# Kernel optimization log

Measured on AMD Instinct MI355X. Metric: run time of the kernel, lower is better.

## Reference

```python
import jax, jax.numpy as jnp
import numpy as np

N_NODES, N_EDGES, D, B, K, M = 100000, 500000, 172, 500, 10, 1000
MSG = 4 * D  # 2*memory_dim + edge_dim + time_dim = 688


def setup_inputs() -> dict:
    ks = jax.random.split(jax.random.key(0), 34)
    rn = lambda k, s, sc=0.05: jax.random.normal(k, s, jnp.float32) * sc
    ri = lambda k, s, hi: jax.random.randint(k, s, 0, hi, dtype=jnp.int32)
    ru = lambda k, s, sc=1000.0: jax.random.uniform(k, s, dtype=jnp.float32) * sc
    return {
        "node_feats": rn(ks[0], (N_NODES, D)),
        "edge_feats": rn(ks[1], (N_EDGES, D)),
        "memory": rn(ks[2], (N_NODES, D)),
        "time_w": rn(ks[3], (D,), 1.0),
        "time_b": rn(ks[4], (D,), 1.0),
        "W_ih": rn(ks[5], (3 * D, MSG)),
        "W_hh": rn(ks[6], (3 * D, D)),
        "b_ih": rn(ks[7], (3 * D,)),
        "b_hh": rn(ks[8], (3 * D,)),
        "lin1_w": rn(ks[9], (2, 3 * D, D)),
        "lin1_b": rn(ks[10], (2, D)),
        "lin2_w": rn(ks[11], (2, 3 * D, D)),
        "lin2_b": rn(ks[12], (2, D)),
        "aff_w1": rn(ks[13], (2 * D, D)),
        "aff_b1": rn(ks[14], (D,)),
        "aff_w2": rn(ks[15], (D, 1)),
        "aff_b2": rn(ks[16], (1,)),
        "dec_w": rn(ks[17], (D, D)),
        "dec_b": rn(ks[18], (D,)),
        "edge_times": ru(ks[19], (B,)),
        "nbr1_t": ru(ks[20], (3 * B, K)),
        "nbr2_t": ru(ks[21], (3 * B * K, K)),
        "msgs": rn(ks[22], (M, MSG)),
        "msg_times": ru(ks[23], (M,)),
        "src": ri(ks[24], (B,), N_NODES),
        "dst": ri(ks[25], (B,), N_NODES),
        "neg": ri(ks[26], (B,), N_NODES),
        "edge_idxs": ri(ks[27], (B,), N_EDGES),
        "nbr1_ids": ri(ks[28], (3 * B, K), N_NODES),
        "nbr1_eidx": ri(ks[29], (3 * B, K), N_EDGES),
        "nbr2_ids": ri(ks[30], (3 * B * K, K), N_NODES),
        "nbr2_eidx": ri(ks[31], (3 * B * K, K), N_EDGES),
        "msg_node_ids": jnp.arange(M, dtype=jnp.int32),  # unique nodes with pending messages
    }


def _time_enc(t, w, b):
    # TGN TimeEncode: cos(t * w + b), broadcast over last dim D
    return jnp.cos(t[..., None] * w + b)


def _gru(x, h, W_ih, W_hh, b_ih, b_hh):
    # torch.nn.GRUCell math
    gi = x @ W_ih.T + b_ih
    gh = h @ W_hh.T + b_hh
    ir, iz, ig = jnp.split(gi, 3, -1)
    hr, hz, hg = jnp.split(gh, 3, -1)
    r = jax.nn.sigmoid(ir + hr)
    z = jax.nn.sigmoid(iz + hz)
    g = jnp.tanh(ig + r * hg)
    return (1.0 - z) * g + z * h


def _agg(l, src_feat, ts, nbr_emb, nbr_t, edge_f, tw, tb, l1w, l1b, l2w, l2b):
    # GraphSumEmbedding.aggregate for layer index l (0-based = n_layer-1)
    dt = _time_enc(ts[:, None] - nbr_t, tw, tb)                 # [N,K,D]
    nf = jnp.concatenate([nbr_emb, dt, edge_f], -1)             # [N,K,3D]
    h = jax.nn.relu((nf @ l1w[l] + l1b[l]).sum(1))              # sum over K neighbors -> [N,D]
    st = _time_enc(jnp.zeros_like(ts), tw, tb)                  # time-embedding of delta 0
    s = jnp.concatenate([h, src_feat, st], -1)                  # [N,3D]
    return s @ l2w[l] + l2b[l]


def reference(node_feats, edge_feats, memory, time_w, time_b, W_ih, W_hh, b_ih, b_hh,
              lin1_w, lin1_b, lin2_w, lin2_b, aff_w1, aff_b1, aff_w2, aff_b2,
              dec_w, dec_b, edge_times, nbr1_t, nbr2_t, msgs, msg_times,
              src, dst, neg, edge_idxs, nbr1_ids, nbr1_eidx, nbr2_ids, nbr2_eidx,
              msg_node_ids):
    b, k = src.shape[0], nbr1_ids.shape[1]
    d = node_feats.shape[1]
    # 1) get_updated_memory: GRU update of nodes with aggregated-last messages, scatter into bank
    h_new = _gru(msgs, memory[msg_node_ids], W_ih, W_hh, b_ih, b_hh)
    mem = memory.at[msg_node_ids].set(h_new)
    feat0 = lambda n: mem[n] + node_feats[n]  # layer-0 embedding = memory + raw features
    # 2) two-layer graph-sum temporal embedding over concat(src,dst,neg)
    nodes = jnp.concatenate([src, dst, neg])                    # [3B]
    ts = jnp.concatenate([edge_times, edge_times, edge_times])  # [3B]
    n1 = nbr1_ids.reshape(-1)                                   # [3B*K]
    ts1 = jnp.repeat(ts, k)                                     # [3B*K]
    emb1 = _agg(0, feat0(n1), ts1, feat0(nbr2_ids), nbr2_t,
                edge_feats[nbr2_eidx], time_w, time_b, lin1_w, lin1_b, lin2_w, lin2_b)
    emb2 = _agg(1, feat0(nodes), ts, emb1.reshape(-1, k, d), nbr1_t,
                edge_feats[nbr1_eidx], time_w, time_b, lin1_w, lin1_b, lin2_w, lin2_b)
    s_emb, d_emb, g_emb = emb2[:b], emb2[b:2 * b], emb2[2 * b:]
    # 3) affinity (MergeLayer) scores + MLP decode + raw feature gather
    def merge(x1, x2):
        h = jax.nn.relu(jnp.concatenate([x1, x2], -1) @ aff_w1 + aff_b1)
        return (h @ aff_w2 + aff_b2).reshape(-1)
    pos_prob = jax.nn.sigmoid(merge(s_emb, d_emb))
    neg_prob = jax.nn.sigmoid(merge(s_emb, g_emb))
    decode = jnp.concatenate([s_emb, d_emb], 0) @ dec_w + dec_b
    raw = jnp.concatenate([node_feats[src], node_feats[dst]], 0)
    return (pos_prob, neg_prob, decode, raw)
```

## Files before the change

### kernel.cpp

```cpp
#include <hip/hip_runtime.h>

#define DD   172
#define TK   516
#define BB   500
#define KK   10
#define MM   1000
#define MSGW 688
#define NR1  1500
#define NR2  15000

__device__ __forceinline__ float sigm(float x){ return 1.f / (1.f + expf(-x)); }

__global__ void k_tr(const float* __restrict__ in, float* __restrict__ out,
                     int R, int C){
  __shared__ float tile[32][33];
  int c0 = blockIdx.x * 32, r0 = blockIdx.y * 32;
  int tx = threadIdx.x, ty = threadIdx.y;
  for (int i = ty; i < 32; i += 8){
    int r = r0 + i, c = c0 + tx;
    if (r < R && c < C) tile[i][tx] = in[(size_t)r*C + c];
  }
  __syncthreads();
  for (int i = ty; i < 32; i += 8){
    int c = c0 + i, r = r0 + tx;
    if (c < C && r < R) out[(size_t)c*R + r] = tile[tx][i];
  }
}

__global__ void k_gru2(const float* __restrict__ msgs, float* memory,
                       const float* __restrict__ WT_ih,
                       const float* __restrict__ WT_hh,
                       const float* __restrict__ b_ih, const float* __restrict__ b_hh,
                       const int* __restrict__ ids){
  int t = threadIdx.x;
  int r0 = blockIdx.x * 2;
  __shared__ __align__(16) float xT[MSGW][2];
  __shared__ __align__(16) float hT[DD][2];
  int s0 = ids[r0], s1 = ids[r0 + 1];
  for (int c = t; c < MSGW; c += 192){
    xT[c][0] = msgs[(size_t)r0*MSGW + c];
    xT[c][1] = msgs[(size_t)(r0+1)*MSGW + c];
  }
  if (t < DD){
    hT[t][0] = memory[(size_t)s0*DD + t];
    hT[t][1] = memory[(size_t)s1*DD + t];
  }
  __syncthreads();
  if (t < DD){
    float gi00 = b_ih[t],      gi01 = gi00;
    float gi10 = b_ih[DD+t],   gi11 = gi10;
    float gi20 = b_ih[2*DD+t], gi21 = gi20;
    #pragma unroll 4
    for (int c = 0; c < MSGW; c++){
      const float* wr = WT_ih + (size_t)c*TK;
      float w0 = wr[t], w1 = wr[DD+t], w2 = wr[2*DD+t];
      float2 xv = *reinterpret_cast<const float2*>(&xT[c][0]);
      gi00 = fmaf(xv.x, w0, gi00); gi01 = fmaf(xv.y, w0, gi01);
      gi10 = fmaf(xv.x, w1, gi10); gi11 = fmaf(xv.y, w1, gi11);
      gi20 = fmaf(xv.x, w2, gi20); gi21 = fmaf(xv.y, w2, gi21);
    }
    float gh00 = b_hh[t],      gh01 = gh00;
    float gh10 = b_hh[DD+t],   gh11 = gh10;
    float gh20 = b_hh[2*DD+t], gh21 = gh20;
    #pragma unroll 4
    for (int c = 0; c < DD; c++){
      const float* wr = WT_hh + (size_t)c*TK;
      float w0 = wr[t], w1 = wr[DD+t], w2 = wr[2*DD+t];
      float2 hv = *reinterpret_cast<const float2*>(&hT[c][0]);
      gh00 = fmaf(hv.x, w0, gh00); gh01 = fmaf(hv.y, w0, gh01);
      gh10 = fmaf(hv.x, w1, gh10); gh11 = fmaf(hv.y, w1, gh11);
      gh20 = fmaf(hv.x, w2, gh20); gh21 = fmaf(hv.y, w2, gh21);
    }
    {
      float r_ = sigm(gi00 + gh00);
      float z  = sigm(gi10 + gh10);
      float g  = tanhf(gi20 + r_*gh20);
      memory[(size_t)s0*DD + t] = (1.f - z)*g + z*hT[t][0];
    }
    {
      float r_ = sigm(gi01 + gh01);
      float z  = sigm(gi11 + gh11);
      float g  = tanhf(gi21 + r_*gh21);
      memory[(size_t)s1*DD + t] = (1.f - z)*g + z*hT[t][1];
    }
  }
}

__global__ void k_c2(const float* __restrict__ time_b, const float* __restrict__ lin2_w,
                     const float* __restrict__ lin2_b, float* __restrict__ consts){
  int l = blockIdx.x, j = threadIdx.x;
  __shared__ float cb[DD];
  if (j < DD) cb[j] = cosf(time_b[j]);
  __syncthreads();
  if (j < DD){
    float acc = lin2_b[(size_t)l*DD + j];
    const float* W = lin2_w + (size_t)l*TK*DD;
    for (int d = 0; d < DD; d++) acc = fmaf(cb[d], W[(size_t)(2*DD + d)*DD + j], acc);
    consts[l*DD + j] = acc;
  }
}

__global__ void k_hop2(const float* __restrict__ nf, const float* __restrict__ ef,
                       const float* __restrict__ mem, const float* __restrict__ tw,
                       const float* __restrict__ tb, const float* __restrict__ et,
                       const float* __restrict__ n2t, const int* __restrict__ n2i,
                       const int* __restrict__ n2e, const int* __restrict__ n1i,
                       const float* __restrict__ l1w, const float* __restrict__ l2w,
                       const float* __restrict__ l1b, const float* __restrict__ consts,
                       float* __restrict__ emb1){
  int t = threadIdx.x;
  int r0 = blockIdx.x * 8;
  __shared__ __align__(16) float S[TK][8];
  __shared__ __align__(16) float H[2*DD][8];
  __shared__ int   I2[8*KK], E2[8*KK], SID[8];
  __shared__ float T2[8*KK];
  if (t < 8*KK){
    int r = r0 + t/KK, k = t % KK;
    I2[t] = n2i[(size_t)r*KK + k];
    E2[t] = n2e[(size_t)r*KK + k];
    T2[t] = n2t[(size_t)r*KK + k];
  }
  if (t >= 96 && t < 104) SID[t-96] = n1i[r0 + (t-96)];
  __syncthreads();
  if (t < DD){
    float w = tw[t], b = tb[t];
    for (int rr = 0; rr < 8; rr++){
      int r = r0 + rr;
      float ts = et[(r/KK) % BB];
      float sn = 0.f, sd = 0.f, se = 0.f;
      #pragma unroll
      for (int k = 0; k < KK; k++){
        int id = I2[rr*KK + k];
        int e  = E2[rr*KK + k];
        float dt = ts - T2[rr*KK + k];
        sn += mem[(size_t)id*DD + t] + nf[(size_t)id*DD + t];
        sd += cosf(dt*w + b);
        se += ef[(size_t)e*DD + t];
      }
      S[t][rr] = sn; S[DD + t][rr] = sd; S[2*DD + t][rr] = se;
      int sid = SID[rr];
      H[DD + t][rr] = mem[(size_t)sid*DD + t] + nf[(size_t)sid*DD + t];
    }
  }
  __syncthreads();
  if (t < DD){
    float acc[8];
    float b10 = 10.f * l1b[t];
    #pragma unroll
    for (int rr = 0; rr < 8; rr++) acc[rr] = b10;
    const float* Wp = l1w + t;
    #pragma unroll 4
    for (int c = 0; c < TK; c++){
      float wv = Wp[(size_t)c*DD];
      float4 a = *reinterpret_cast<const float4*>(&S[c][0]);
      float4 q = *reinterpret_cast<const float4*>(&S[c][4]);
      acc[0] = fmaf(a.x, wv, acc[0]); acc[1] = fmaf(a.y, wv, acc[1]);
      acc[2] = fmaf(a.z, wv, acc[2]); acc[3] = fmaf(a.w, wv, acc[3]);
      acc[4] = fmaf(q.x, wv, acc[4]); acc[5] = fmaf(q.y, wv, acc[5]);
      acc[6] = fmaf(q.z, wv, acc[6]); acc[7] = fmaf(q.w, wv, acc[7]);
    }
    #pragma unroll
    for (int rr = 0; rr < 8; rr++) H[t][rr] = fmaxf(acc[rr], 0.f);
  }
  __syncthreads();
  if (t < DD){
    float acc[8];
    float c2 = consts[t];
    #pragma unroll
    for (int rr = 0; rr < 8; rr++) acc[rr] = c2;
    const float* Wp = l2w + t;
    #pragma unroll 4
    for (int c = 0; c < 2*DD; c++){
      float wv = Wp[(size_t)c*DD];
      float4 a = *reinterpret_cast<const float4*>(&H[c][0]);
      float4 q = *reinterpret_cast<const float4*>(&H[c][4]);
      acc[0] = fmaf(a.x, wv, acc[0]); acc[1] = fmaf(a.y, wv, acc[1]);
      acc[2] = fmaf(a.z, wv, acc[2]); acc[3] = fmaf(a.w, wv, acc[3]);
      acc[4] = fmaf(q.x, wv, acc[4]); acc[5] = fmaf(q.y, wv, acc[5]);
      acc[6] = fmaf(q.z, wv, acc[6]); acc[7] = fmaf(q.w, wv, acc[7]);
    }
    #pragma unroll
    for (int rr = 0; rr < 8; rr++) emb1[(size_t)(r0+rr)*DD + t] = acc[rr];
  }
}

__global__ void k_hop1(const float* __restrict__ nf, const float* __restrict__ ef,
                       const float* __restrict__ mem, const float* __restrict__ tw,
                       const float* __restrict__ tb, const float* __restrict__ et,
                       const float* __restrict__ n1t, const int* __restrict__ n1e,
                       const int* __restrict__ src, const int* __restrict__ dst,
                       const int* __restrict__ neg, const float* __restrict__ emb1,
                       const float* __restrict__ l1w, const float* __restrict__ l2w,
                       const float* __restrict__ l1b, const float* __restrict__ consts,
                       float* __restrict__ emb2){
  int t = threadIdx.x;
  int r0 = blockIdx.x * 8;
  __shared__ __align__(16) float S[TK][8];
  __shared__ __align__(16) float H[2*DD][8];
  __shared__ int   E1[8*KK], SID[8];
  __shared__ float T1[8*KK];
  if (t < 8*KK){
    int q = r0 + t/KK; if (q >= NR1) q = NR1 - 1;
    int k = t % KK;
    E1[t] = n1e[(size_t)q*KK + k];
    T1[t] = n1t[(size_t)q*KK + k];
  }
  if (t >= 96 && t < 104){
    int q = r0 + (t - 96); if (q >= NR1) q = NR1 - 1;
    SID[t-96] = (q < BB) ? src[q] : (q < 2*BB ? dst[q - BB] : neg[q - 2*BB]);
  }
  __syncthreads();
  if (t < DD){
    float w = tw[t], b = tb[t];
    for (int rr = 0; rr < 8; rr++){
      int q = r0 + rr; if (q >= NR1) q = NR1 - 1;
      float ts = et[q % BB];
      float sn = 0.f, sd = 0.f, se = 0.f;
      #pragma unroll
      for (int k = 0; k < KK; k++){
        int e = E1[rr*KK + k];
        float dt = ts - T1[rr*KK + k];
        sn += emb1[((size_t)q*KK + k)*DD + t];
        sd += cosf(dt*w + b);
        se += ef[(size_t)e*DD + t];
      }
      S[t][rr] = sn; S[DD + t][rr] = sd; S[2*DD + t][rr] = se;
      int sid = SID[rr];
      H[DD + t][rr] = mem[(size_t)sid*DD + t] + nf[(size_t)sid*DD + t];
    }
  }
  __syncthreads();
  if (t < DD){
    float acc[8];
    float b10 = 10.f * l1b[t];
    #pragma unroll
    for (int rr = 0; rr < 8; rr++) acc[rr] = b10;
    const float* Wp = l1w + t;
    #pragma unroll 4
    for (int c = 0; c < TK; c++){
      float wv = Wp[(size_t)c*DD];
      float4 a = *reinterpret_cast<const float4*>(&S[c][0]);
      float4 q = *reinterpret_cast<const float4*>(&S[c][4]);
      acc[0] = fmaf(a.x, wv, acc[0]); acc[1] = fmaf(a.y, wv, acc[1]);
      acc[2] = fmaf(a.z, wv, acc[2]); acc[3] = fmaf(a.w, wv, acc[3]);
      acc[4] = fmaf(q.x, wv, acc[4]); acc[5] = fmaf(q.y, wv, acc[5]);
      acc[6] = fmaf(q.z, wv, acc[6]); acc[7] = fmaf(q.w, wv, acc[7]);
    }
    #pragma unroll
    for (int rr = 0; rr < 8; rr++) H[t][rr] = fmaxf(acc[rr], 0.f);
  }
  __syncthreads();
  if (t < DD){
    float acc[8];
    float c2 = consts[DD + t];
    #pragma unroll
    for (int rr = 0; rr < 8; rr++) acc[rr] = c2;
    const float* Wp = l2w + t;
    #pragma unroll 4
    for (int c = 0; c < 2*DD; c++){
      float wv = Wp[(size_t)c*DD];
      float4 a = *reinterpret_cast<const float4*>(&H[c][0]);
      float4 q = *reinterpret_cast<const float4*>(&H[c][4]);
      acc[0] = fmaf(a.x, wv, acc[0]); acc[1] = fmaf(a.y, wv, acc[1]);
      acc[2] = fmaf(a.z, wv, acc[2]); acc[3] = fmaf(a.w, wv, acc[3]);
      acc[4] = fmaf(q.x, wv, acc[4]); acc[5] = fmaf(q.y, wv, acc[5]);
      acc[6] = fmaf(q.z, wv, acc[6]); acc[7] = fmaf(q.w, wv, acc[7]);
    }
    #pragma unroll
    for (int rr = 0; rr < 8; rr++){
      int q = r0 + rr;
      if (q < NR1) emb2[(size_t)q*DD + t] = acc[rr];
    }
  }
}

__global__ void k_merge(const float* __restrict__ emb2, const float* __restrict__ aff_w1,
                        const float* __restrict__ aff_b1, const float* __restrict__ aff_w2,
                        const float* __restrict__ aff_b2, float* __restrict__ out){
  int idx = blockIdx.x;
  int which = idx / BB, r = idx % BB;
  int t = threadIdx.x;
  __shared__ float x1[DD], x2[DD], hs[DD];
  if (t < DD){
    x1[t] = emb2[(size_t)r*DD + t];
    x2[t] = emb2[(size_t)(which == 0 ? BB + r : 2*BB + r)*DD + t];
  }
  __syncthreads();
  if (t < DD){
    float acc = aff_b1[t];
    for (int c = 0; c < DD; c++) acc = fmaf(x1[c], aff_w1[(size_t)c*DD + t], acc);
    for (int c = 0; c < DD; c++) acc = fmaf(x2[c], aff_w1[(size_t)(DD + c)*DD + t], acc);
    hs[t] = fmaxf(acc, 0.f) * aff_w2[t];
  }
  __syncthreads();
  if (t < 64){
    float s = hs[t] + hs[t + 64];
    if (t < DD - 128) s += hs[t + 128];
    #pragma unroll
    for (int off = 32; off > 0; off >>= 1) s += __shfl_down(s, off, 64);
    if (t == 0) out[which*BB + r] = sigm(s + aff_b2[0]);
  }
}

__global__ void k_dec(const float* __restrict__ emb2, const float* __restrict__ dec_w,
                      const float* __restrict__ dec_b, float* __restrict__ out){
  int t = threadIdx.x;
  int r0 = blockIdx.x * 8;
  if (t < DD){
    float acc[8];
    float bj = dec_b[t];
    #pragma unroll
    for (int rr = 0; rr < 8; rr++) acc[rr] = bj;
    for (int c = 0; c < DD; c++){
      float wv = dec_w[(size_t)c*DD + t];
      #pragma unroll
      for (int rr = 0; rr < 8; rr++)
        acc[rr] = fmaf(emb2[(size_t)(r0+rr)*DD + c], wv, acc[rr]);
    }
    #pragma unroll
    for (int rr = 0; rr < 8; rr++) out[(size_t)(r0+rr)*DD + t] = acc[rr];
  }
}

__global__ void k_raw(const float* __restrict__ node_feats, const int* __restrict__ src,
                      const int* __restrict__ dst, float* __restrict__ out){
  int q = blockIdx.x, t = threadIdx.x;
  int id = (q < BB) ? src[q] : dst[q - BB];
  if (t < DD) out[(size_t)q*DD + t] = node_feats[(size_t)id*DD + t];
}

extern "C" void kernel_launch(void* const* d_in, const int* in_sizes, int n_in,
                              void* d_out, int out_size, void* d_ws, size_t ws_size,
                              hipStream_t stream){
  (void)in_sizes; (void)n_in; (void)out_size; (void)ws_size;
  const float* node_feats = (const float*)d_in[0];
  const float* edge_feats = (const float*)d_in[1];
  float*       memory     = (float*)d_in[2];
  const float* time_w     = (const float*)d_in[3];
  const float* time_b     = (const float*)d_in[4];
  const float* W_ih       = (const float*)d_in[5];
  const float* W_hh       = (const float*)d_in[6];
  const float* b_ih       = (const float*)d_in[7];
  const float* b_hh       = (const float*)d_in[8];
  const float* lin1_w     = (const float*)d_in[9];
  const float* lin1_b     = (const float*)d_in[10];
  const float* lin2_w     = (const float*)d_in[11];
  const float* lin2_b     = (const float*)d_in[12];
  const float* aff_w1     = (const float*)d_in[13];
  const float* aff_b1     = (const float*)d_in[14];
  const float* aff_w2     = (const float*)d_in[15];
  const float* aff_b2     = (const float*)d_in[16];
  const float* dec_w      = (const float*)d_in[17];
  const float* dec_b      = (const float*)d_in[18];
  const float* edge_times = (const float*)d_in[19];
  const float* nbr1_t     = (const float*)d_in[20];
  const float* nbr2_t     = (const float*)d_in[21];
  const float* msgs       = (const float*)d_in[22];
  const int* src        = (const int*)d_in[24];
  const int* dst        = (const int*)d_in[25];
  const int* neg        = (const int*)d_in[26];
  const int* nbr1_ids   = (const int*)d_in[28];
  const int* nbr1_eidx  = (const int*)d_in[29];
  const int* nbr2_ids   = (const int*)d_in[30];
  const int* nbr2_eidx  = (const int*)d_in[31];
  const int* msg_ids    = (const int*)d_in[32];
  float* out = (float*)d_out;

  float* consts = (float*)d_ws;
  float* emb1   = (float*)((char*)d_ws + 2048);
  float* emb2   = emb1 + (size_t)NR2*DD;
  float* WT_ih  = emb1;
  float* WT_hh  = WT_ih + (size_t)MSGW*TK;

  k_tr  <<<dim3((MSGW+31)/32, (TK+31)/32), dim3(32,8), 0, stream>>>(W_ih, WT_ih, TK, MSGW);
  k_tr  <<<dim3((DD+31)/32,   (TK+31)/32), dim3(32,8), 0, stream>>>(W_hh, WT_hh, TK, DD);
  k_gru2<<<MM/2, 192, 0, stream>>>(msgs, memory, WT_ih, WT_hh, b_ih, b_hh, msg_ids);
  k_c2  <<<2, 192, 0, stream>>>(time_b, lin2_w, lin2_b, consts);
  k_hop2<<<NR2/8, 192, 0, stream>>>(node_feats, edge_feats, memory, time_w, time_b,
                                    edge_times, nbr2_t, nbr2_ids, nbr2_eidx, nbr1_ids,
                                    lin1_w, lin2_w, lin1_b, consts, emb1);
  k_hop1<<<(NR1+7)/8, 192, 0, stream>>>(node_feats, edge_feats, memory, time_w, time_b,
                                        edge_times, nbr1_t, nbr1_eidx, src, dst, neg,
                                        emb1, lin1_w + (size_t)TK*DD, lin2_w + (size_t)TK*DD,
                                        lin1_b + DD, consts, emb2);
  k_merge<<<2*BB, 192, 0, stream>>>(emb2, aff_w1, aff_b1, aff_w2, aff_b2, out);
  k_dec <<<MM/8, 192, 0, stream>>>(emb2, dec_w, dec_b, out + 2*BB);
  k_raw <<<MM, 192, 0, stream>>>(node_feats, src, dst, out + 2*BB + (size_t)MM*DD);
}
```

Baseline: 993.7 us.

## Batch weight loads ahead of FMAs, shrink shared memory, stage decoder inputs

Result: faster. 938.5 us (-5.6%).

```diff
diff --git a/kernel.cpp b/kernel.cpp
--- a/kernel.cpp
+++ b/kernel.cpp
@@ -50,26 +50,38 @@
     float gi00 = b_ih[t],      gi01 = gi00;
     float gi10 = b_ih[DD+t],   gi11 = gi10;
     float gi20 = b_ih[2*DD+t], gi21 = gi20;
-    #pragma unroll 4
-    for (int c = 0; c < MSGW; c++){
-      const float* wr = WT_ih + (size_t)c*TK;
-      float w0 = wr[t], w1 = wr[DD+t], w2 = wr[2*DD+t];
-      float2 xv = *reinterpret_cast<const float2*>(&xT[c][0]);
-      gi00 = fmaf(xv.x, w0, gi00); gi01 = fmaf(xv.y, w0, gi01);
-      gi10 = fmaf(xv.x, w1, gi10); gi11 = fmaf(xv.y, w1, gi11);
-      gi20 = fmaf(xv.x, w2, gi20); gi21 = fmaf(xv.y, w2, gi21);
+    for (int c0 = 0; c0 < MSGW; c0 += 8){
+      float w0[8], w1[8], w2[8]; float2 xv[8];
+      #pragma unroll
+      for (int u = 0; u < 8; u++){
+        const float* wr = WT_ih + (size_t)(c0+u)*TK;
+        w0[u] = wr[t]; w1[u] = wr[DD+t]; w2[u] = wr[2*DD+t];
+        xv[u] = *reinterpret_cast<const float2*>(&xT[c0+u][0]);
+      }
+      #pragma unroll
+      for (int u = 0; u < 8; u++){
+        gi00 = fmaf(xv[u].x, w0[u], gi00); gi01 = fmaf(xv[u].y, w0[u], gi01);
+        gi10 = fmaf(xv[u].x, w1[u], gi10); gi11 = fmaf(xv[u].y, w1[u], gi11);
+        gi20 = fmaf(xv[u].x, w2[u], gi20); gi21 = fmaf(xv[u].y, w2[u], gi21);
+      }
     }
     float gh00 = b_hh[t],      gh01 = gh00;
     float gh10 = b_hh[DD+t],   gh11 = gh10;
     float gh20 = b_hh[2*DD+t], gh21 = gh20;
-    #pragma unroll 4
-    for (int c = 0; c < DD; c++){
-      const float* wr = WT_hh + (size_t)c*TK;
-      float w0 = wr[t], w1 = wr[DD+t], w2 = wr[2*DD+t];
-      float2 hv = *reinterpret_cast<const float2*>(&hT[c][0]);
-      gh00 = fmaf(hv.x, w0, gh00); gh01 = fmaf(hv.y, w0, gh01);
-      gh10 = fmaf(hv.x, w1, gh10); gh11 = fmaf(hv.y, w1, gh11);
-      gh20 = fmaf(hv.x, w2, gh20); gh21 = fmaf(hv.y, w2, gh21);
+    for (int c0 = 0; c0 < DD; c0 += 4){
+      float w0[4], w1[4], w2[4]; float2 hv[4];
+      #pragma unroll
+      for (int u = 0; u < 4; u++){
+        const float* wr = WT_hh + (size_t)(c0+u)*TK;
+        w0[u] = wr[t]; w1[u] = wr[DD+t]; w2[u] = wr[2*DD+t];
+        hv[u] = *reinterpret_cast<const float2*>(&hT[c0+u][0]);
+      }
+      #pragma unroll
+      for (int u = 0; u < 4; u++){
+        gh00 = fmaf(hv[u].x, w0[u], gh00); gh01 = fmaf(hv[u].y, w0[u], gh01);
+        gh10 = fmaf(hv[u].x, w1[u], gh10); gh11 = fmaf(hv[u].y, w1[u], gh11);
+        gh20 = fmaf(hv[u].x, w2[u], gh20); gh21 = fmaf(hv[u].y, w2[u], gh21);
+      }
     }
     {
       float r_ = sigm(gi00 + gh00);
@@ -94,8 +106,14 @@
   __syncthreads();
   if (j < DD){
     float acc = lin2_b[(size_t)l*DD + j];
-    const float* W = lin2_w + (size_t)l*TK*DD;
-    for (int d = 0; d < DD; d++) acc = fmaf(cb[d], W[(size_t)(2*DD + d)*DD + j], acc);
+    const float* W = lin2_w + (size_t)l*TK*DD + (size_t)2*DD*DD + j;
+    for (int d0 = 0; d0 < DD; d0 += 4){
+      float wv[4];
+      #pragma unroll
+      for (int u = 0; u < 4; u++) wv[u] = W[(size_t)(d0+u)*DD];
+      #pragma unroll
+      for (int u = 0; u < 4; u++) acc = fmaf(cb[d0+u], wv[u], acc);
+    }
     consts[l*DD + j] = acc;
   }
 }
@@ -111,7 +129,7 @@
   int t = threadIdx.x;
   int r0 = blockIdx.x * 8;
   __shared__ __align__(16) float S[TK][8];
-  __shared__ __align__(16) float H[2*DD][8];
+  __shared__ __align__(16) float Hhi[DD][8];
   __shared__ int   I2[8*KK], E2[8*KK], SID[8];
   __shared__ float T2[8*KK];
   if (t < 8*KK){
@@ -127,57 +145,97 @@
     for (int rr = 0; rr < 8; rr++){
       int r = r0 + rr;
       float ts = et[(r/KK) % BB];
-      float sn = 0.f, sd = 0.f, se = 0.f;
+      float vm[KK], vn[KK], ve[KK], vt[KK];
       #pragma unroll
       for (int k = 0; k < KK; k++){
         int id = I2[rr*KK + k];
         int e  = E2[rr*KK + k];
-        float dt = ts - T2[rr*KK + k];
-        sn += mem[(size_t)id*DD + t] + nf[(size_t)id*DD + t];
-        sd += cosf(dt*w + b);
-        se += ef[(size_t)e*DD + t];
+        vm[k] = mem[(size_t)id*DD + t];
+        vn[k] = nf[(size_t)id*DD + t];
+        ve[k] = ef[(size_t)e*DD + t];
+        vt[k] = T2[rr*KK + k];
+      }
+      float sn = 0.f, sd = 0.f, se = 0.f;
+      #pragma unroll
+      for (int k = 0; k < KK; k++){
+        sn += vm[k] + vn[k];
+        sd += cosf((ts - vt[k])*w + b);
+        se += ve[k];
       }
       S[t][rr] = sn; S[DD + t][rr] = sd; S[2*DD + t][rr] = se;
       int sid = SID[rr];
-      H[DD + t][rr] = mem[(size_t)sid*DD + t] + nf[(size_t)sid*DD + t];
-    }
-  }
-  __syncthreads();
-  if (t < DD){
-    float acc[8];
+      Hhi[t][rr] = mem[(size_t)sid*DD + t] + nf[(size_t)sid*DD + t];
+    }
+  }
+  __syncthreads();
+  float acc[8];
+  if (t < DD){
     float b10 = 10.f * l1b[t];
     #pragma unroll
     for (int rr = 0; rr < 8; rr++) acc[rr] = b10;
     const float* Wp = l1w + t;
-    #pragma unroll 4
-    for (int c = 0; c < TK; c++){
-      float wv = Wp[(size_t)c*DD];
-      float4 a = *reinterpret_cast<const float4*>(&S[c][0]);
-      float4 q = *reinterpret_cast<const float4*>(&S[c][4]);
-      acc[0] = fmaf(a.x, wv, acc[0]); acc[1] = fmaf(a.y, wv, acc[1]);
-      acc[2] = fmaf(a.z, wv, acc[2]); acc[3] = fmaf(a.w, wv, acc[3]);
-      acc[4] = fmaf(q.x, wv, acc[4]); acc[5] = fmaf(q.y, wv, acc[5]);
-      acc[6] = fmaf(q.z, wv, acc[6]); acc[7] = fmaf(q.w, wv, acc[7]);
-    }
-    #pragma unroll
-    for (int rr = 0; rr < 8; rr++) H[t][rr] = fmaxf(acc[rr], 0.f);
-  }
-  __syncthreads();
-  if (t < DD){
-    float acc[8];
+    for (int c0 = 0; c0 < TK; c0 += 4){
+      float wv[4]; float4 a[4], q[4];
+      #pragma unroll
+      for (int u = 0; u < 4; u++){
+        wv[u] = Wp[(size_t)(c0+u)*DD];
+        a[u] = *reinterpret_cast<const float4*>(&S[c0+u][0]);
+        q[u] = *reinterpret_cast<const float4*>(&S[c0+u][4]);
+      }
+      #pragma unroll
+      for (int u = 0; u < 4; u++){
+        acc[0]=fmaf(a[u].x,wv[u],acc[0]); acc[1]=fmaf(a[u].y,wv[u],acc[1]);
+        acc[2]=fmaf(a[u].z,wv[u],acc[2]); acc[3]=fmaf(a[u].w,wv[u],acc[3]);
+        acc[4]=fmaf(q[u].x,wv[u],acc[4]); acc[5]=fmaf(q[u].y,wv[u],acc[5]);
+        acc[6]=fmaf(q[u].z,wv[u],acc[6]); acc[7]=fmaf(q[u].w,wv[u],acc[7]);
+      }
+    }
+  }
+  __syncthreads();
+  if (t < DD){
+    float4 h0, h1;
+    h0.x=fmaxf(acc[0],0.f); h0.y=fmaxf(acc[1],0.f); h0.z=fmaxf(acc[2],0.f); h0.w=fmaxf(acc[3],0.f);
+    h1.x=fmaxf(acc[4],0.f); h1.y=fmaxf(acc[5],0.f); h1.z=fmaxf(acc[6],0.f); h1.w=fmaxf(acc[7],0.f);
+    *reinterpret_cast<float4*>(&S[t][0]) = h0;
+    *reinterpret_cast<float4*>(&S[t][4]) = h1;
+  }
+  __syncthreads();
+  if (t < DD){
     float c2 = consts[t];
     #pragma unroll
     for (int rr = 0; rr < 8; rr++) acc[rr] = c2;
     const float* Wp = l2w + t;
-    #pragma unroll 4
-    for (int c = 0; c < 2*DD; c++){
-      float wv = Wp[(size_t)c*DD];
-      float4 a = *reinterpret_cast<const float4*>(&H[c][0]);
-      float4 q = *reinterpret_cast<const float4*>(&H[c][4]);
-      acc[0] = fmaf(a.x, wv, acc[0]); acc[1] = fmaf(a.y, wv, acc[1]);
-      acc[2] = fmaf(a.z, wv, acc[2]); acc[3] = fmaf(a.w, wv, acc[3]);
-      acc[4] = fmaf(q.x, wv, acc[4]); acc[5] = fmaf(q.y, wv, acc[5]);
-      acc[6] = fmaf(q.z, wv, acc[6]); acc[7] = fmaf(q.w, wv, acc[7]);
+    for (int c0 = 0; c0 < DD; c0 += 4){
+      float wv[4]; float4 a[4], q[4];
+      #pragma unroll
+      for (int u = 0; u < 4; u++){
+        wv[u] = Wp[(size_t)(c0+u)*DD];
+        a[u] = *reinterpret_cast<const float4*>(&S[c0+u][0]);
+        q[u] = *reinterpret_cast<const float4*>(&S[c0+u][4]);
+      }
+      #pragma unroll
+      for (int u = 0; u < 4; u++){
+        acc[0]=fmaf(a[u].x,wv[u],acc[0]); acc[1]=fmaf(a[u].y,wv[u],acc[1]);
+        acc[2]=fmaf(a[u].z,wv[u],acc[2]); acc[3]=fmaf(a[u].w,wv[u],acc[3]);
+        acc[4]=fmaf(q[u].x,wv[u],acc[4]); acc[5]=fmaf(q[u].y,wv[u],acc[5]);
+        acc[6]=fmaf(q[u].z,wv[u],acc[6]); acc[7]=fmaf(q[u].w,wv[u],acc[7]);
+      }
+    }
+    for (int c0 = 0; c0 < DD; c0 += 4){
+      float wv[4]; float4 a[4], q[4];
+      #pragma unroll
+      for (int u = 0; u < 4; u++){
+        wv[u] = Wp[(size_t)(DD+c0+u)*DD];
+        a[u] = *reinterpret_cast<const float4*>(&Hhi[c0+u][0]);
+        q[u] = *reinterpret_cast<const float4*>(&Hhi[c0+u][4]);
+      }
+      #pragma unroll
+      for (int u = 0; u < 4; u++){
+        acc[0]=fmaf(a[u].x,wv[u],acc[0]); acc[1]=fmaf(a[u].y,wv[u],acc[1]);
+        acc[2]=fmaf(a[u].z,wv[u],acc[2]); acc[3]=fmaf(a[u].w,wv[u],acc[3]);
+        acc[4]=fmaf(q[u].x,wv[u],acc[4]); acc[5]=fmaf(q[u].y,wv[u],acc[5]);
+        acc[6]=fmaf(q[u].z,wv[u],acc[6]); acc[7]=fmaf(q[u].w,wv[u],acc[7]);
+      }
     }
     #pragma unroll
     for (int rr = 0; rr < 8; rr++) emb1[(size_t)(r0+rr)*DD + t] = acc[rr];
@@ -196,7 +254,7 @@
   int t = threadIdx.x;
   int r0 = blockIdx.x * 8;
   __shared__ __align__(16) float S[TK][8];
-  __shared__ __align__(16) float H[2*DD][8];
+  __shared__ __align__(16) float Hhi[DD][8];
   __shared__ int   E1[8*KK], SID[8];
   __shared__ float T1[8*KK];
   if (t < 8*KK){
@@ -215,56 +273,95 @@
     for (int rr = 0; rr < 8; rr++){
       int q = r0 + rr; if (q >= NR1) q = NR1 - 1;
       float ts = et[q % BB];
-      float sn = 0.f, sd = 0.f, se = 0.f;
+      float v1[KK], ve[KK], vt[KK];
       #pragma unroll
       for (int k = 0; k < KK; k++){
         int e = E1[rr*KK + k];
-        float dt = ts - T1[rr*KK + k];
-        sn += emb1[((size_t)q*KK + k)*DD + t];
-        sd += cosf(dt*w + b);
-        se += ef[(size_t)e*DD + t];
+        v1[k] = emb1[((size_t)q*KK + k)*DD + t];
+        ve[k] = ef[(size_t)e*DD + t];
+        vt[k] = T1[rr*KK + k];
+      }
+      float sn = 0.f, sd = 0.f, se = 0.f;
+      #pragma unroll
+      for (int k = 0; k < KK; k++){
+        sn += v1[k];
+        sd += cosf((ts - vt[k])*w + b);
+        se += ve[k];
       }
       S[t][rr] = sn; S[DD + t][rr] = sd; S[2*DD + t][rr] = se;
       int sid = SID[rr];
-      H[DD + t][rr] = mem[(size_t)sid*DD + t] + nf[(size_t)sid*DD + t];
-    }
-  }
-  __syncthreads();
-  if (t < DD){
-    float acc[8];
+      Hhi[t][rr] = mem[(size_t)sid*DD + t] + nf[(size_t)sid*DD + t];
+    }
+  }
+  __syncthreads();
+  float acc[8];
+  if (t < DD){
     float b10 = 10.f * l1b[t];
     #pragma unroll
     for (int rr = 0; rr < 8; rr++) acc[rr] = b10;
     const float* Wp = l1w + t;
-    #pragma unroll 4
-    for (int c = 0; c < TK; c++){
-      float wv = Wp[(size_t)c*DD];
-      float4 a = *reinterpret_cast<const float4*>(&S[c][0]);
-      float4 q = *reinterpret_cast<const float4*>(&S[c][4]);
-      acc[0] = fmaf(a.x, wv, acc[0]); acc[1] = fmaf(a.y, wv, acc[1]);
-      acc[2] = fmaf(a.z, wv, acc[2]); acc[3] = fmaf(a.w, wv, acc[3]);
-      acc[4] = fmaf(q.x, wv, acc[4]); acc[5] = fmaf(q.y, wv, acc[5]);
-      acc[6] = fmaf(q.z, wv, acc[6]); acc[7] = fmaf(q.w, wv, acc[7]);
-    }
-    #pragma unroll
-    for (int rr = 0; rr < 8; rr++) H[t][rr] = fmaxf(acc[rr], 0.f);
-  }
-  __syncthreads();
-  if (t < DD){
-    float acc[8];
+    for (int c0 = 0; c0 < TK; c0 += 4){
+      float wv[4]; float4 a[4], q[4];
+      #pragma unroll
+      for (int u = 0; u < 4; u++){
+        wv[u] = Wp[(size_t)(c0+u)*DD];
+        a[u] = *reinterpret_cast<const float4*>(&S[c0+u][0]);
+        q[u] = *reinterpret_cast<const float4*>(&S[c0+u][4]);
+      }
+      #pragma unroll
+      for (int u = 0; u < 4; u++){
+        acc[0]=fmaf(a[u].x,wv[u],acc[0]); acc[1]=fmaf(a[u].y,wv[u],acc[1]);
+        acc[2]=fmaf(a[u].z,wv[u],acc[2]); acc[3]=fmaf(a[u].w,wv[u],acc[3]);
+        acc[4]=fmaf(q[u].x,wv[u],acc[4]); acc[5]=fmaf(q[u].y,wv[u],acc[5]);
+        acc[6]=fmaf(q[u].z,wv[u],acc[6]); acc[7]=fmaf(q[u].w,wv[u],acc[7]);
+      }
+    }
+  }
+  __syncthreads();
+  if (t < DD){
+    float4 h0, h1;
+    h0.x=fmaxf(acc[0],0.f); h0.y=fmaxf(acc[1],0.f); h0.z=fmaxf(acc[2],0.f); h0.w=fmaxf(acc[3],0.f);
+    h1.x=fmaxf(acc[4],0.f); h1.y=fmaxf(acc[5],0.f); h1.z=fmaxf(acc[6],0.f); h1.w=fmaxf(acc[7],0.f);
+    *reinterpret_cast<float4*>(&S[t][0]) = h0;
+    *reinterpret_cast<float4*>(&S[t][4]) = h1;
+  }
+  __syncthreads();
+  if (t < DD){
     float c2 = consts[DD + t];
     #pragma unroll
     for (int rr = 0; rr < 8; rr++) acc[rr] = c2;
     const float* Wp = l2w + t;
-    #pragma unroll 4
-    for (int c = 0; c < 2*DD; c++){
-      float wv = Wp[(size_t)c*DD];
-      float4 a = *reinterpret_cast<const float4*>(&H[c][0]);
-      float4 q = *reinterpret_cast<const float4*>(&H[c][4]);
-      acc[0] = fmaf(a.x, wv, acc[0]); acc[1] = fmaf(a.y, wv, acc[1]);
-      acc[2] = fmaf(a.z, wv, acc[2]); acc[3] = fmaf(a.w, wv, acc[3]);
-      acc[4] = fmaf(q.x, wv, acc[4]); acc[5] = fmaf(q.y, wv, acc[5]);
-      acc[6] = fmaf(q.z, wv, acc[6]); acc[7] = fmaf(q.w, wv, acc[7]);
+    for (int c0 = 0; c0 < DD; c0 += 4){
+      float wv[4]; float4 a[4], q[4];
+      #pragma unroll
+      for (int u = 0; u < 4; u++){
+        wv[u] = Wp[(size_t)(c0+u)*DD];
+        a[u] = *reinterpret_cast<const float4*>(&S[c0+u][0]);
+        q[u] = *reinterpret_cast<const float4*>(&S[c0+u][4]);
+      }
+      #pragma unroll
+      for (int u = 0; u < 4; u++){
+        acc[0]=fmaf(a[u].x,wv[u],acc[0]); acc[1]=fmaf(a[u].y,wv[u],acc[1]);
+        acc[2]=fmaf(a[u].z,wv[u],acc[2]); acc[3]=fmaf(a[u].w,wv[u],acc[3]);
+        acc[4]=fmaf(q[u].x,wv[u],acc[4]); acc[5]=fmaf(q[u].y,wv[u],acc[5]);
+        acc[6]=fmaf(q[u].z,wv[u],acc[6]); acc[7]=fmaf(q[u].w,wv[u],acc[7]);
+      }
+    }
+    for (int c0 = 0; c0 < DD; c0 += 4){
+      float wv[4]; float4 a[4], q[4];
+      #pragma unroll
+      for (int u = 0; u < 4; u++){
+        wv[u] = Wp[(size_t)(DD+c0+u)*DD];
+        a[u] = *reinterpret_cast<const float4*>(&Hhi[c0+u][0]);
+        q[u] = *reinterpret_cast<const float4*>(&Hhi[c0+u][4]);
+      }
+      #pragma unroll
+      for (int u = 0; u < 4; u++){
+        acc[0]=fmaf(a[u].x,wv[u],acc[0]); acc[1]=fmaf(a[u].y,wv[u],acc[1]);
+        acc[2]=fmaf(a[u].z,wv[u],acc[2]); acc[3]=fmaf(a[u].w,wv[u],acc[3]);
+        acc[4]=fmaf(q[u].x,wv[u],acc[4]); acc[5]=fmaf(q[u].y,wv[u],acc[5]);
+        acc[6]=fmaf(q[u].z,wv[u],acc[6]); acc[7]=fmaf(q[u].w,wv[u],acc[7]);
+      }
     }
     #pragma unroll
     for (int rr = 0; rr < 8; rr++){
@@ -288,8 +385,21 @@
   __syncthreads();
   if (t < DD){
     float acc = aff_b1[t];
-    for (int c = 0; c < DD; c++) acc = fmaf(x1[c], aff_w1[(size_t)c*DD + t], acc);
-    for (int c = 0; c < DD; c++) acc = fmaf(x2[c], aff_w1[(size_t)(DD + c)*DD + t], acc);
+    const float* W1 = aff_w1 + t;
+    for (int c0 = 0; c0 < DD; c0 += 4){
+      float wv[4];
+      #pragma unroll
+      for (int u = 0; u < 4; u++) wv[u] = W1[(size_t)(c0+u)*DD];
+      #pragma unroll
+      for (int u = 0; u < 4; u++) acc = fmaf(x1[c0+u], wv[u], acc);
+    }
+    for (int c0 = 0; c0 < DD; c0 += 4){
+      float wv[4];
+      #pragma unroll
+      for (int u = 0; u < 4; u++) wv[u] = W1[(size_t)(DD+c0+u)*DD];
+      #pragma unroll
+      for (int u = 0; u < 4; u++) acc = fmaf(x2[c0+u], wv[u], acc);
+    }
     hs[t] = fmaxf(acc, 0.f) * aff_w2[t];
   }
   __syncthreads();
@@ -306,16 +416,25 @@
                       const float* __restrict__ dec_b, float* __restrict__ out){
   int t = threadIdx.x;
   int r0 = blockIdx.x * 8;
+  __shared__ __align__(16) float E[8*DD];
+  for (int i = t; i < 8*DD; i += 192) E[i] = emb2[(size_t)r0*DD + i];
+  __syncthreads();
   if (t < DD){
     float acc[8];
     float bj = dec_b[t];
     #pragma unroll
     for (int rr = 0; rr < 8; rr++) acc[rr] = bj;
-    for (int c = 0; c < DD; c++){
-      float wv = dec_w[(size_t)c*DD + t];
-      #pragma unroll
-      for (int rr = 0; rr < 8; rr++)
-        acc[rr] = fmaf(emb2[(size_t)(r0+rr)*DD + c], wv, acc[rr]);
+    const float* Wp = dec_w + t;
+    for (int c0 = 0; c0 < DD; c0 += 4){
+      float wv[4];
+      #pragma unroll
+      for (int u = 0; u < 4; u++) wv[u] = Wp[(size_t)(c0+u)*DD];
+      #pragma unroll
+      for (int u = 0; u < 4; u++){
+        #pragma unroll
+        for (int rr = 0; rr < 8; rr++)
+          acc[rr] = fmaf(E[rr*DD + c0+u], wv[u], acc[rr]);
+      }
     }
     #pragma unroll
     for (int rr = 0; rr < 8; rr++) out[(size_t)(r0+rr)*DD + t] = acc[rr];
```
